# Kernel tuning notes

Measured on AMD Instinct MI355X. Metric: run time of the kernel, lower is better.

## Reference

```python
import jax, jax.numpy as jnp
import numpy as np

LEAK = 0.2
EPS_LN = 1e-5   # nn.LayerNorm default
EPS_IN = 1e-5   # nn.InstanceNorm2d default
EPS_D = 1e-8    # demodulation eps


def _leaky(x):
    return jnp.where(x >= 0, x, LEAK * x)


def _layernorm(s, g, b):
    mu = s.mean(-1, keepdims=True)
    v = ((s - mu) ** 2).mean(-1, keepdims=True)
    return (s - mu) / jnp.sqrt(v + EPS_LN) * g + b


def _instnorm(x):
    # per (b, c) normalization over HW, no affine (InstanceNorm2d default)
    mu = x.mean((2, 3), keepdims=True)
    v = ((x - mu) ** 2).mean((2, 3), keepdims=True)
    return (x - mu) / jnp.sqrt(v + EPS_IN)


def _conv(x, wt, pad):
    # x: [B,C,H,W], wt: [O,I,k,k]
    return jax.lax.conv_general_dilated(
        x, wt, (1, 1), [(pad, pad), (pad, pad)],
        dimension_numbers=('NCHW', 'OIHW', 'NCHW'))


def _modconv(x, w, wt, scale, mw, mb, lg, lb, asw, asb, abw, abb, demod):
    # style -> per-sample per-in-channel modulation
    s = _leaky(_layernorm(w @ mw.T + mb, lg, lb))              # [b, in]
    wb = wt[None] * (s[:, None, :, None, None] * scale[None])  # [b, O, I, k, k]
    # AdaIN on the input (use_adain=True in this block)
    sc = (w @ asw.T + asb)[:, :, None, None]
    bi = (w @ abw.T + abb)[:, :, None, None]
    x = sc * _instnorm(x) + bi
    if demod:
        d = jax.lax.rsqrt(jnp.sum(wb * wb, axis=(2, 3, 4)) + EPS_D)  # [b, O]
        wb = wb * d[:, :, None, None, None]
    pad = wt.shape[-1] // 2
    # per-sample conv == groups=b grouped conv in the torch original
    return jax.vmap(lambda xi, wi: _conv(xi[None], wi, pad)[0])(x, wb)


def _upsample2x(x):
    B, C, H, W = x.shape
    # bilinear, half-pixel centers == torch align_corners=False
    return jax.image.resize(x, (B, C, 2 * H, 2 * W), 'bilinear')


def setup_inputs() -> dict:
    key = jax.random.key(0)
    ks = iter(jax.random.split(key, 64))
    B, Cin, Cout, L, H = 8, 128, 64, 512, 128
    rn = lambda shape, s=1.0: jax.random.normal(next(ks), shape, jnp.float32) * s
    lin = 1.0 / float(np.sqrt(L))
    return dict(
        x=rn((B, Cin, H, H)), w=rn((B, L)),
        w1=rn((Cout, Cin, 3, 3), 0.02), sc1=jnp.ones((1, Cin, 1, 1), jnp.float32),
        m1_w=rn((Cin, L), lin), m1_b=jnp.zeros((Cin,), jnp.float32),
        ln1_g=jnp.ones((Cin,), jnp.float32), ln1_b=jnp.zeros((Cin,), jnp.float32),
        a1_sw=rn((Cin, L), lin), a1_sb=jnp.zeros((Cin,), jnp.float32),
        a1_bw=rn((Cin, L), lin), a1_bb=jnp.zeros((Cin,), jnp.float32),
        w25=rn((4, Cout, Cout, 3, 3), 0.02), sc25=jnp.ones((4, 1, Cout, 1, 1), jnp.float32),
        m25_w=rn((4, Cout, L), lin), m25_b=jnp.zeros((4, Cout), jnp.float32),
        ln25_g=jnp.ones((4, Cout), jnp.float32), ln25_b=jnp.zeros((4, Cout), jnp.float32),
        a25_sw=rn((4, Cout, L), lin), a25_sb=jnp.zeros((4, Cout), jnp.float32),
        a25_bw=rn((4, Cout, L), lin), a25_bb=jnp.zeros((4, Cout), jnp.float32),
        wr=rn((3, Cout, 1, 1), 0.02), scr=jnp.ones((1, Cout, 1, 1), jnp.float32),
        mr_w=rn((Cout, L), lin), mr_b=jnp.zeros((Cout,), jnp.float32),
        lnr_g=jnp.ones((Cout,), jnp.float32), lnr_b=jnp.zeros((Cout,), jnp.float32),
        ar_sw=rn((Cout, L), lin), ar_sb=jnp.zeros((Cout,), jnp.float32),
        ar_bw=rn((Cout, L), lin), ar_bb=jnp.zeros((Cout,), jnp.float32),
        sk_w=rn((Cout, Cin, 1, 1), 0.02), sk_b=jnp.zeros((Cout,), jnp.float32),
    )


def reference(x, w, w1, sc1, m1_w, m1_b, ln1_g, ln1_b, a1_sw, a1_sb, a1_bw, a1_bb,
              w25, sc25, m25_w, m25_b, ln25_g, ln25_b, a25_sw, a25_sb, a25_bw, a25_bb,
              wr, scr, mr_w, mr_b, lnr_g, lnr_b, ar_sw, ar_sb, ar_bw, ar_bb,
              sk_w, sk_b):
    x = _upsample2x(x)
    skip = _conv(x, sk_w, 0) + sk_b[None, :, None, None]
    h = _leaky(_modconv(x, w, w1, sc1, m1_w, m1_b, ln1_g, ln1_b,
                        a1_sw, a1_sb, a1_bw, a1_bb, True))
    for i in range(4):  # conv2..conv5, identical structure
        h = _leaky(_modconv(h, w, w25[i], sc25[i], m25_w[i], m25_b[i],
                            ln25_g[i], ln25_b[i], a25_sw[i], a25_sb[i],
                            a25_bw[i], a25_bb[i], True))
    h = h + skip
    rgb = _modconv(h, w, wr, scr, mr_w, mr_b, lnr_g, lnr_b,
                   ar_sw, ar_sb, ar_bw, ar_bb, False)
    return h, rgb
```

## Files before the change

kernel.cpp:

```cpp
#include <hip/hip_runtime.h>
#include <cstdint>

#define LEAK 0.2f

typedef __attribute__((ext_vector_type(8))) short bf16x8;
typedef __attribute__((ext_vector_type(4))) float f32x4;

__device__ __forceinline__ float leaky(float v){ return v >= 0.f ? v : LEAK*v; }

__device__ __forceinline__ uint32_t f32_to_bf16_rne(float v){
    uint32_t u = __float_as_uint(v);
    return (u + 0x7fffu + ((u >> 16) & 1u)) >> 16;
}
__device__ __forceinline__ uint32_t split_pack(float v){
    uint32_t u = __float_as_uint(v);
    uint32_t hb = (u + 0x7fffu + ((u >> 16) & 1u)) & 0xffff0000u;
    float lof = v - __uint_as_float(hb);
    uint32_t lo = f32_to_bf16_rne(lof);
    return (hb >> 16) | (lo << 16);
}

__global__ __launch_bounds__(128)
void style_all_kernel(const float* __restrict__ w,
    const float* __restrict__ m1_w,  const float* __restrict__ m1_b,
    const float* __restrict__ ln1_g, const float* __restrict__ ln1_b,
    const float* __restrict__ a1_sw, const float* __restrict__ a1_sb,
    const float* __restrict__ a1_bw, const float* __restrict__ a1_bb,
    const float* __restrict__ sc1,
    const float* __restrict__ m25_w,  const float* __restrict__ m25_b,
    const float* __restrict__ ln25_g, const float* __restrict__ ln25_b,
    const float* __restrict__ a25_sw, const float* __restrict__ a25_sb,
    const float* __restrict__ a25_bw, const float* __restrict__ a25_bb,
    const float* __restrict__ sc25,
    const float* __restrict__ mr_w,  const float* __restrict__ mr_b,
    const float* __restrict__ lnr_g, const float* __restrict__ lnr_b,
    const float* __restrict__ ar_sw, const float* __restrict__ ar_sb,
    const float* __restrict__ ar_bw, const float* __restrict__ ar_bb,
    const float* __restrict__ scr,
    float* __restrict__ sty)
{
    int l = blockIdx.x >> 3;
    int b = blockIdx.x & 7;
    const float *mw, *mb, *lng, *lnb, *asw, *asb, *abw, *abb, *sc;
    int Cin;
    if (l == 0) {
        mw=m1_w; mb=m1_b; lng=ln1_g; lnb=ln1_b;
        asw=a1_sw; asb=a1_sb; abw=a1_bw; abb=a1_bb; sc=sc1; Cin=128;
    } else if (l <= 4) {
        int j = l - 1;
        mw=m25_w+(size_t)j*32768; mb=m25_b+j*64; lng=ln25_g+j*64; lnb=ln25_b+j*64;
        asw=a25_sw+(size_t)j*32768; asb=a25_sb+j*64;
        abw=a25_bw+(size_t)j*32768; abb=a25_bb+j*64; sc=sc25+j*64; Cin=64;
    } else {
        mw=mr_w; mb=mr_b; lng=lnr_g; lnb=lnr_b;
        asw=ar_sw; asb=ar_sb; abw=ar_bw; abb=ar_bb; sc=scr; Cin=64;
    }
    float* out_sm  = sty + l*3072;
    float* out_asc = out_sm + 1024;
    float* out_abi = out_sm + 2048;

    __shared__ float wl[512];
    __shared__ float red[128];
    int tid = threadIdx.x;
    for (int j = tid; j < 512; j += 128) wl[j] = w[b*512 + j];
    __syncthreads();

    float t = 0.f, ascv = 0.f, abiv = 0.f;
    if (tid < Cin) {
        const float* r1 = mw  + (size_t)tid*512;
        const float* r2 = asw + (size_t)tid*512;
        const float* r3 = abw + (size_t)tid*512;
        for (int j = 0; j < 512; ++j) {
            float wj = wl[j];
            t    = fmaf(wj, r1[j], t);
            ascv = fmaf(wj, r2[j], ascv);
            abiv = fmaf(wj, r3[j], abiv);
        }
        t += mb[tid]; ascv += asb[tid]; abiv += abb[tid];
    }
    red[tid] = (tid < Cin) ? t : 0.f;
    __syncthreads();
    for (int s = 64; s > 0; s >>= 1) { if (tid < s) red[tid] += red[tid+s]; __syncthreads(); }
    float mu = red[0] / (float)Cin;
    __syncthreads();
    float dv = (tid < Cin) ? (t - mu) : 0.f;
    red[tid] = dv*dv;
    __syncthreads();
    for (int s = 64; s > 0; s >>= 1) { if (tid < s) red[tid] += red[tid+s]; __syncthreads(); }
    float var = red[0] / (float)Cin;
    float rstd = rsqrtf(var + 1e-5f);
    if (tid < Cin) {
        float sln = (t - mu) * rstd * lng[tid] + lnb[tid];
        sln = leaky(sln);
        out_sm[b*128 + tid]  = sln * sc[tid];
        out_asc[b*128 + tid] = ascv;
        out_abi[b*128 + tid] = abiv;
    }
}

__global__ __launch_bounds__(256)
void upsample_pack_kernel(const float* __restrict__ x, uint32_t* __restrict__ Up,
                          float* __restrict__ sums)
{
    int bid = blockIdx.x;
    int b = bid >> 8, y = bid & 255;
    int tid = threadIdx.x;
    int c = tid & 15, pg = tid >> 4;
    int q = y >> 1; int rlo, rhi; float wlo, whi;
    if (y & 1) { rlo = q; rhi = (q+1 < 127) ? q+1 : 127; wlo = 0.75f; whi = 0.25f; }
    else       { rlo = (q-1 > 0) ? q-1 : 0; rhi = q;     wlo = 0.25f; whi = 0.75f; }
    __shared__ float xs[2][16][129];
    __shared__ float red2[2][4][16];
    for (int cg = 0; cg < 8; ++cg) {
        __syncthreads();
        for (int e = tid; e < 4096; e += 256) {
            int row = e >> 11, cc = (e >> 7) & 15, px = e & 127;
            xs[row][cc][px] = x[((size_t)(b*128 + cg*16 + cc) << 14) + (row ? rhi : rlo)*128 + px];
        }
        __syncthreads();
        float s = 0.f, sq = 0.f;
        uint32_t* base = Up + ((((size_t)(b*8 + cg)*256 + y)*256))*16 + c;
        #pragma unroll
        for (int k = 0; k < 16; ++k) {
            int px = pg*16 + k;
            int m = px >> 1;
            float v;
            if (px & 1) {
                int m2 = (m+1 < 127) ? m+1 : 127;
                float vc = wlo*xs[0][c][m]  + whi*xs[1][c][m];
                float vr = wlo*xs[0][c][m2] + whi*xs[1][c][m2];
                v = 0.75f*vc + 0.25f*vr;
            } else {
                int m0 = (m-1 > 0) ? m-1 : 0;
                float vl = wlo*xs[0][c][m0] + whi*xs[1][c][m0];
                float vc = wlo*xs[0][c][m]  + whi*xs[1][c][m];
                v = 0.25f*vl + 0.75f*vc;
            }
            s += v; sq += v*v;
            base[(size_t)px*16] = split_pack(v);
        }
        s  += __shfl_xor(s, 16);  s  += __shfl_xor(s, 32);
        sq += __shfl_xor(sq, 16); sq += __shfl_xor(sq, 32);
        int wid = tid >> 6;
        if ((tid & 63) < 16) { red2[0][wid][c] = s; red2[1][wid][c] = sq; }
        __syncthreads();
        if (tid < 16) {
            float S = red2[0][0][tid] + red2[0][1][tid] + red2[0][2][tid] + red2[0][3][tid];
            float Q = red2[1][0][tid] + red2[1][1][tid] + red2[1][2][tid] + red2[1][3][tid];
            atomicAdd(&sums[(b*128 + cg*16 + tid)*2],     S);
            atomicAdd(&sums[(b*128 + cg*16 + tid)*2 + 1], Q);
        }
    }
}

__global__ __launch_bounds__(256)
void packskip_kernel(const float* __restrict__ skw, uint16_t* __restrict__ skp)
{
    int e = blockIdx.x*256 + threadIdx.x;
    if (e >= 8192) return;
    int o = e >> 7, i = e & 127;
    uint32_t pk = split_pack(skw[e]);
    int ic = i >> 4, cl = i & 15, cg = cl >> 2, j2 = (cl & 3)*2;
    uint16_t* dst = skp + ic*2048 + (o >> 4)*512 + cg*128 + (o & 15)*8 + j2;
    dst[0] = (uint16_t)(pk & 0xffffu);
    dst[1] = (uint16_t)(pk >> 16);
}

template<int CIN>
__global__ __launch_bounds__(CIN)
void packw_kernel(const float* __restrict__ wt, const float* __restrict__ sty,
                  const float* __restrict__ sums,
                  uint16_t* __restrict__ wp, float* __restrict__ bias9,
                  float* __restrict__ dmodL)
{
    int b = blockIdx.x >> 6;
    int o = blockIdx.x & 63;
    int i = threadIdx.x;

    float sm = sty[b*128 + i];
    float av = sty[1024 + b*128 + i];
    float bv = sty[2048 + b*128 + i];
    float s0 = sums[(b*CIN + i)*2], s1 = sums[(b*CIN + i)*2 + 1];
    float m = s0 * (1.f/65536.f);
    float var = s1 * (1.f/65536.f) - m*m;
    float r = rsqrtf((var > 0.f ? var : 0.f) + 1e-5f);
    float A  = sm * av * r;
    float Bv = sm * (bv - av*m*r);

    const float* wrow = wt + ((size_t)o*CIN + i)*9;
    float c9[9];
    #pragma unroll
    for (int k = 0; k < 9; ++k) c9[k] = wrow[k];

    const int NCH = CIN/16;
    int ic = i >> 4, cl = i & 15, cg = cl >> 2, j2 = (cl & 3)*2;
    uint16_t* wpb = wp + ((size_t)b*NCH + ic)*18432;
    float wsq = 0.f;
    #pragma unroll
    for (int k = 0; k < 9; ++k) { wsq = fmaf(c9[k], c9[k], wsq); }
    #pragma unroll
    for (int k = 0; k < 9; ++k) {
        float wv = c9[k] * A;
        uint32_t pk = split_pack(wv);
        uint16_t* dst = wpb + k*2048 + (o >> 4)*512 + cg*128 + (o & 15)*8 + j2;
        dst[0] = (uint16_t)(pk & 0xffffu);
        dst[1] = (uint16_t)(pk >> 16);
    }

    float colS[3][3];
    #pragma unroll
    for (int ky = 0; ky < 3; ++ky) {
        colS[ky][0] = c9[ky*3+1] + c9[ky*3+2];
        colS[ky][1] = c9[ky*3+0] + c9[ky*3+1] + c9[ky*3+2];
        colS[ky][2] = c9[ky*3+0] + c9[ky*3+1];
    }
    float part[9];
    #pragma unroll
    for (int rx = 0; rx < 3; ++rx) {
        part[0*3+rx] = colS[1][rx] + colS[2][rx];
        part[1*3+rx] = colS[0][rx] + colS[1][rx] + colS[2][rx];
        part[2*3+rx] = colS[0][rx] + colS[1][rx];
    }
    __shared__ float red[10][CIN];
    #pragma unroll
    for (int t = 0; t < 9; ++t) red[t][i] = part[t] * Bv;
    red[9][i] = wsq * sm * sm;
    __syncthreads();
    for (int s = CIN/2; s > 0; s >>= 1) {
        if (i < s) {
            #pragma unroll
            for (int t = 0; t < 10; ++t) red[t][i] += red[t][i + s];
        }
        __syncthreads();
    }
    if (i < 9) bias9[((size_t)(b*64 + o))*9 + i] = red[i][0];
    if (i == 9) dmodL[b*64 + o] = rsqrtf(red[9][0] + 1e-8f);
}

template<int CIN, int MODE, bool SKIP>
__global__ __launch_bounds__(512)
void conv_mfma_kernel(const uint32_t* __restrict__ inPair,
                      const uint16_t* __restrict__ Wp,
                      const float* __restrict__ bias9,
                      const float* __restrict__ dmod,
                      const uint16_t* __restrict__ skp,
                      const float* __restrict__ skb,
                      float* __restrict__ skipOut,
                      uint32_t* __restrict__ outPair,
                      float* __restrict__ outF32,
                      float* __restrict__ statsH)
{
    __shared__ __align__(16) unsigned char LDS[41600];
    const int tid = threadIdx.x;
    const int lane = tid & 63, wv = tid >> 6;
    const int rw = wv >> 2, oq = wv & 3;

    int bid = blockIdx.x;
    bid = (bid & 7) * 256 + (bid >> 3);
    const int xh = bid & 1, yb = (bid >> 1) & 127, b = bid >> 8;
    const int y0 = yb*2, x0 = xh*128;

    union U8 { uint32_t u[4]; bf16x8 v; };

    f32x4 acc[8];
    f32x4 accS[SKIP ? 8 : 1];
    #pragma unroll
    for (int q = 0; q < 8; ++q) acc[q] = (f32x4){0.f, 0.f, 0.f, 0.f};
    if constexpr (SKIP) {
        #pragma unroll
        for (int q = 0; q < 8; ++q) accS[q] = (f32x4){0.f, 0.f, 0.f, 0.f};
    }

    const int NCH = CIN/16;
    for (int ic = 0; ic < NCH; ++ic) {
        for (int e = tid; e < 2080; e += 512) {
            int part = e & 3;
            int pr = e >> 2;
            int px = pr % 130, row = pr / 130;
            int yy = y0 - 1 + row, xx = x0 - 1 + px;
            uint4 v = {0u, 0u, 0u, 0u};
            if (yy >= 0 && yy < 256 && xx >= 0 && xx < 256)
                v = *reinterpret_cast<const uint4*>(
                    inPair + ((((size_t)b*NCH + ic)*256 + yy)*256 + xx)*16 + part*4);
            *reinterpret_cast<uint4*>(LDS + row*10400 + px*80 + part*16) = v;
        }
        __syncthreads();
        const uint16_t* wbase = Wp + ((size_t)b*NCH + ic)*18432
                              + oq*512 + (lane >> 4)*128 + (lane & 15)*8;
        #pragma unroll
        for (int tap = 0; tap < 9; ++tap) {
            const int dy1 = tap/3, dxm = tap % 3;
            uint4 wv4 = *reinterpret_cast<const uint4*>(wbase + tap*2048);
            U8 wa, wb;
            #pragma unroll
            for (int q = 0; q < 4; ++q) {
                uint32_t ww = (&wv4.x)[q];
                wa.u[q] = __builtin_amdgcn_perm(ww, ww, 0x01000100u);
                wb.u[q] = __builtin_amdgcn_perm(ww, ww, 0x03020302u);
            }
            U8 sa, sb;
            if constexpr (SKIP) {
                if (tap == 4) {
                    uint4 sfrag = *reinterpret_cast<const uint4*>(
                        skp + ic*2048 + oq*512 + (lane >> 4)*128 + (lane & 15)*8);
                    #pragma unroll
                    for (int q = 0; q < 4; ++q) {
                        uint32_t ww = (&sfrag.x)[q];
                        sa.u[q] = __builtin_amdgcn_perm(ww, ww, 0x01000100u);
                        sb.u[q] = __builtin_amdgcn_perm(ww, ww, 0x03020302u);
                    }
                }
            }
            const int rowbase = (rw + dy1)*10400 + (lane >> 4)*16 + ((lane & 15) + dxm)*80;
            #pragma unroll
            for (int xf = 0; xf < 8; ++xf) {
                bf16x8 bf = *reinterpret_cast<const bf16x8*>(LDS + rowbase + xf*1280);
                acc[xf] = __builtin_amdgcn_mfma_f32_16x16x32_bf16(wa.v, bf, acc[xf], 0, 0, 0);
                acc[xf] = __builtin_amdgcn_mfma_f32_16x16x32_bf16(wb.v, bf, acc[xf], 0, 0, 0);
                if constexpr (SKIP) {
                    if (tap == 4) {
                        accS[xf] = __builtin_amdgcn_mfma_f32_16x16x32_bf16(sa.v, bf, accS[xf], 0, 0, 0);
                        accS[xf] = __builtin_amdgcn_mfma_f32_16x16x32_bf16(sb.v, bf, accS[xf], 0, 0, 0);
                    }
                }
            }
        }
        __syncthreads();
    }

    const int y = y0 + rw;
    const int ry = (y == 0) ? 0 : ((y == 255) ? 2 : 1);
    float dv4[4], bmid[4], bl[4], br[4], skb4[4];
    #pragma unroll
    for (int r2 = 0; r2 < 4; ++r2) {
        int o = oq*16 + (lane >> 4)*4 + r2;
        dv4[r2] = dmod[b*64 + o];
        const float* bp = bias9 + ((size_t)(b*64 + o))*9 + ry*3;
        bmid[r2] = bp[1];
        bl[r2] = bmid[r2]; br[r2] = bmid[r2];
        if (x0 == 0   && (lane & 15) == 0)  bl[r2] = bp[0];
        if (x0 == 128 && (lane & 15) == 15) br[r2] = bp[2];
        if constexpr (SKIP) skb4[r2] = skb[o];
    }

    float s4[4] = {0.f,0.f,0.f,0.f}, q4[4] = {0.f,0.f,0.f,0.f};
    #pragma unroll
    for (int xf = 0; xf < 8; ++xf) {
        #pragma unroll
        for (int r2 = 0; r2 < 4; ++r2) {
            float bias = (xf == 0) ? bl[r2] : ((xf == 7) ? br[r2] : bmid[r2]);
            float v = (acc[xf][r2] + bias) * dv4[r2];
            v = leaky(v);
            acc[xf][r2] = v;
            if (MODE != 2) { s4[r2] += v; q4[r2] += v*v; }
        }
    }

    if constexpr (SKIP) {
        #pragma unroll
        for (int xf = 0; xf < 8; ++xf) {
            #pragma unroll
            for (int r2 = 0; r2 < 4; ++r2) {
                int o = oq*16 + (lane >> 4)*4 + r2;
                size_t addr = ((size_t)(b*64 + o))*65536 + (size_t)y*256 + x0 + xf*16 + (lane & 15);
                skipOut[addr] = accS[xf][r2] + skb4[r2];
            }
        }
    }

    if constexpr (MODE == 2) {
        #pragma unroll
        for (int xf = 0; xf < 8; ++xf) {
            #pragma unroll
            for (int r2 = 0; r2 < 4; ++r2) {
                int o = oq*16 + (lane >> 4)*4 + r2;
                size_t addr = ((size_t)(b*64 + o))*65536 + (size_t)y*256 + x0 + xf*16 + (lane & 15);
                float v = acc[xf][r2] + outF32[addr];
                outF32[addr] = v;
                s4[r2] += v; q4[r2] += v*v;
            }
        }
    }

    #pragma unroll
    for (int r2 = 0; r2 < 4; ++r2) {
        #pragma unroll
        for (int w = 1; w < 16; w <<= 1) {
            s4[r2] += __shfl_xor(s4[r2], w);
            q4[r2] += __shfl_xor(q4[r2], w);
        }
    }
    if ((lane & 15) == 0) {
        #pragma unroll
        for (int r2 = 0; r2 < 4; ++r2) {
            int o = oq*16 + (lane >> 4)*4 + r2;
            atomicAdd(&statsH[(b*64 + o)*2],     s4[r2]);
            atomicAdd(&statsH[(b*64 + o)*2 + 1], q4[r2]);
        }
    }

    if constexpr (MODE != 2) {
        uint32_t* outb = outPair + ((((size_t)b*4 + oq)*256 + y)*256 + x0)*16 + (lane >> 4)*4;
        #pragma unroll
        for (int xf = 0; xf < 8; ++xf) {
            int px = xf*16 + (lane & 15);
            uint4 pk4;
            pk4.x = split_pack(acc[xf][0]);
            pk4.y = split_pack(acc[xf][1]);
            pk4.z = split_pack(acc[xf][2]);
            pk4.w = split_pack(acc[xf][3]);
            *reinterpret_cast<uint4*>(outb + (size_t)px*16) = pk4;
        }
    }
}

__global__ __launch_bounds__(256)
void rgb_kernel(const float* __restrict__ h, const float* __restrict__ wr,
                const float* __restrict__ sty, const float* __restrict__ sums,
                float* __restrict__ rgb)
{
    __shared__ float A[64], Bc[64];
    __shared__ float wl[192];
    int bid = blockIdx.x;
    int b = bid >> 7;
    int px0 = (bid & 127) * 512;
    int tid = threadIdx.x;
    if (tid < 64) {
        float smv = sty[b*128 + tid];
        float av  = sty[1024 + b*128 + tid];
        float bv  = sty[2048 + b*128 + tid];
        float s0 = sums[(b*64 + tid)*2], s1 = sums[(b*64 + tid)*2 + 1];
        float m = s0 * (1.f/65536.f);
        float var = s1 * (1.f/65536.f) - m*m;
        float r = rsqrtf((var > 0.f ? var : 0.f) + 1e-5f);
        A[tid]  = smv * av * r;
        Bc[tid] = smv * (bv - av*m*r);
    }
    if (tid < 192) wl[tid] = wr[tid];
    __syncthreads();
    int pix = px0 + tid*2;
    const float* hp = h + (size_t)b*64*65536 + pix;
    float a0[3] = {0,0,0}, a1[3] = {0,0,0};
    for (int i = 0; i < 64; ++i) {
        float2 v = *reinterpret_cast<const float2*>(hp + (size_t)i*65536);
        float xi0 = fmaf(A[i], v.x, Bc[i]);
        float xi1 = fmaf(A[i], v.y, Bc[i]);
        #pragma unroll
        for (int o = 0; o < 3; ++o) {
            float wv = wl[o*64 + i];
            a0[o] = fmaf(wv, xi0, a0[o]);
            a1[o] = fmaf(wv, xi1, a1[o]);
        }
    }
    float* rp = rgb + (size_t)b*3*65536 + pix;
    #pragma unroll
    for (int o = 0; o < 3; ++o)
        *reinterpret_cast<float2*>(rp + (size_t)o*65536) = make_float2(a0[o], a1[o]);
}

extern "C" void kernel_launch(void* const* d_in, const int* in_sizes, int n_in,
                              void* d_out, int out_size, void* d_ws, size_t ws_size,
                              hipStream_t stream)
{
    const float* x     = (const float*)d_in[0];
    const float* w     = (const float*)d_in[1];
    const float* w1    = (const float*)d_in[2];
    const float* sc1   = (const float*)d_in[3];
    const float* m1_w  = (const float*)d_in[4];
    const float* m1_b  = (const float*)d_in[5];
    const float* ln1_g = (const float*)d_in[6];
    const float* ln1_b = (const float*)d_in[7];
    const float* a1_sw = (const float*)d_in[8];
    const float* a1_sb = (const float*)d_in[9];
    const float* a1_bw = (const float*)d_in[10];
    const float* a1_bb = (const float*)d_in[11];
    const float* w25   = (const float*)d_in[12];
    const float* sc25  = (const float*)d_in[13];
    const float* m25_w = (const float*)d_in[14];
    const float* m25_b = (const float*)d_in[15];
    const float* ln25_g= (const float*)d_in[16];
    const float* ln25_b= (const float*)d_in[17];
    const float* a25_sw= (const float*)d_in[18];
    const float* a25_sb= (const float*)d_in[19];
    const float* a25_bw= (const float*)d_in[20];
    const float* a25_bb= (const float*)d_in[21];
    const float* wr    = (const float*)d_in[22];
    const float* scr   = (const float*)d_in[23];
    const float* mr_w  = (const float*)d_in[24];
    const float* mr_b  = (const float*)d_in[25];
    const float* lnr_g = (const float*)d_in[26];
    const float* lnr_b = (const float*)d_in[27];
    const float* ar_sw = (const float*)d_in[28];
    const float* ar_sb = (const float*)d_in[29];
    const float* ar_bw = (const float*)d_in[30];
    const float* ar_bb = (const float*)d_in[31];
    const float* sk_w  = (const float*)d_in[32];
    const float* sk_b  = (const float*)d_in[33];

    float* outp    = (float*)d_out;
    float* h_out   = outp;
    float* rgb_out = outp + (size_t)33554432;

    uint8_t* ws = (uint8_t*)d_ws;
    uint32_t*  Upair  = (uint32_t*)(ws + 0);
    uint32_t*  hpB    = (uint32_t*)(ws + 0);
    uint32_t*  hpA    = (uint32_t*)(ws + 268435456ull);
    uint16_t*  WpBase = (uint16_t*)(ws + 402653184ull);
    float*     sty    = (float*)(ws + 409731072ull);
    float*     dmod   = (float*)(ws + 409804800ull);
    float*     stats  = (float*)(ws + 409815040ull);
    float*     bias9  = (float*)(ws + 409843712ull);
    uint16_t*  skp    = (uint16_t*)(ws + 409935872ull);

    float* sumsU = stats;
    float* st1   = stats + 2048;
    float* st2   = stats + 3072;
    float* st3   = stats + 4096;
    float* st4   = stats + 5120;
    float* st5   = stats + 6144;

    uint16_t* Wp1 = WpBase;
    uint16_t* Wp2 = WpBase + 1179648;
    uint16_t* Wp3 = Wp2 + 589824;
    uint16_t* Wp4 = Wp3 + 589824;
    uint16_t* Wp5 = Wp4 + 589824;

    hipMemsetAsync(stats, 0, 28672, stream);

    style_all_kernel<<<48,128,0,stream>>>(w,
        m1_w, m1_b, ln1_g, ln1_b, a1_sw, a1_sb, a1_bw, a1_bb, sc1,
        m25_w, m25_b, ln25_g, ln25_b, a25_sw, a25_sb, a25_bw, a25_bb, sc25,
        mr_w, mr_b, lnr_g, lnr_b, ar_sw, ar_sb, ar_bw, ar_bb, scr,
        sty);

    packskip_kernel<<<32,256,0,stream>>>(sk_w, skp);

    upsample_pack_kernel<<<2048,256,0,stream>>>(x, Upair, sumsU);

    packw_kernel<128><<<512,128,0,stream>>>(w1, sty, sumsU, Wp1, bias9, dmod);
    conv_mfma_kernel<128,1,true><<<2048,512,0,stream>>>(Upair, Wp1, bias9, dmod,
                                                        skp, sk_b, h_out,
                                                        hpA, nullptr, st1);
    packw_kernel<64><<<512,64,0,stream>>>(w25, sty + 3072, st1, Wp2, bias9 + 4608, dmod + 512);
    conv_mfma_kernel<64,1,false><<<2048,512,0,stream>>>(hpA, Wp2, bias9 + 4608, dmod + 512,
                                                        nullptr, nullptr, nullptr,
                                                        hpB, nullptr, st2);
    packw_kernel<64><<<512,64,0,stream>>>(w25 + 36864, sty + 2*3072, st2, Wp3, bias9 + 2*4608, dmod + 2*512);
    conv_mfma_kernel<64,1,false><<<2048,512,0,stream>>>(hpB, Wp3, bias9 + 2*4608, dmod + 2*512,
                                                        nullptr, nullptr, nullptr,
                                                        hpA, nullptr, st3);
    packw_kernel<64><<<512,64,0,stream>>>(w25 + 2*36864, sty + 3*3072, st3, Wp4, bias9 + 3*4608, dmod + 3*512);
    conv_mfma_kernel<64,1,false><<<2048,512,0,stream>>>(hpA, Wp4, bias9 + 3*4608, dmod + 3*512,
                                                        nullptr, nullptr, nullptr,
                                                        hpB, nullptr, st4);
    packw_kernel<64><<<512,64,0,stream>>>(w25 + 3*36864, sty + 4*3072, st4, Wp5, bias9 + 4*4608, dmod + 4*512);
    conv_mfma_kernel<64,2,false><<<2048,512,0,stream>>>(hpB, Wp5, bias9 + 4*4608, dmod + 4*512,
                                                        nullptr, nullptr, nullptr,
                                                        nullptr, h_out, st5);

    rgb_kernel<<<1024,256,0,stream>>>(h_out, wr, sty + 5*3072, st5, rgb_out);
}
```

Before: 1.325 ms.

## Add dedicated mid-layer conv kernel with 2-row tiles and multi-fragment register blocking

Adds a specialized conv kernel for the four 64-channel mid layers. Each block handles two rows by half-width, and each wave accumulates a 4x2 grid of MFMA fragments, so each weight load and LDS B-fragment is reused across more outputs. The input halo is staged per 16-channel group into padded LDS. The cost is more accumulator registers and possible occupancy loss at 512 threads, plus a changed block-to-tile mapping.

```diff
diff --git a/kernel.cpp b/kernel.cpp
--- a/kernel.cpp
+++ b/kernel.cpp
@@ -410,6 +410,175 @@
             pk4.z = split_pack(acc[xf][2]);
             pk4.w = split_pack(acc[xf][3]);
             *reinterpret_cast<uint4*>(outb + (size_t)px*16) = pk4;
+        }
+    }
+}
+
+template<int MODE>
+__global__ __launch_bounds__(512)
+void conv_mid_kernel(const uint32_t* __restrict__ inPair,
+                     const uint16_t* __restrict__ Wp,
+                     const float* __restrict__ bias9,
+                     const float* __restrict__ dmod,
+                     uint32_t* __restrict__ outPair,
+                     float* __restrict__ outF32,
+                     float* __restrict__ statsH)
+{
+    __shared__ __align__(16) unsigned char LDS[41600];
+    const int tid = threadIdx.x;
+    const int lane = tid & 63, wvi = tid >> 6;
+    const int rw = wvi >> 2, xh = (wvi >> 1) & 1, oh = wvi & 1;
+
+    int bid = blockIdx.x;
+    bid = (bid & 7) * 256 + (bid >> 3);
+    const int xhb = bid & 1, yb = (bid >> 1) & 127, b = bid >> 8;
+    const int y0 = yb*2, x0 = xhb*128;
+
+    union U8 { uint32_t u[4]; bf16x8 v; };
+
+    f32x4 acc[4][2];
+    #pragma unroll
+    for (int xfl = 0; xfl < 4; ++xfl) {
+        acc[xfl][0] = (f32x4){0.f, 0.f, 0.f, 0.f};
+        acc[xfl][1] = (f32x4){0.f, 0.f, 0.f, 0.f};
+    }
+
+    for (int ic = 0; ic < 4; ++ic) {
+        for (int e = tid; e < 2080; e += 512) {
+            int part = e & 3;
+            int pr = e >> 2;
+            int px = pr % 130, row = pr / 130;
+            int yy = y0 - 1 + row, xx = x0 - 1 + px;
+            uint4 v = {0u, 0u, 0u, 0u};
+            if (yy >= 0 && yy < 256 && xx >= 0 && xx < 256)
+                v = *reinterpret_cast<const uint4*>(
+                    inPair + ((((size_t)b*4 + ic)*256 + yy)*256 + xx)*16 + part*4);
+            *reinterpret_cast<uint4*>(LDS + row*10400 + px*80 + part*16) = v;
+        }
+        __syncthreads();
+        const uint16_t* wbase = Wp + ((size_t)b*4 + ic)*18432
+                              + (lane >> 4)*128 + (lane & 15)*8;
+        #pragma unroll
+        for (int tap = 0; tap < 9; ++tap) {
+            const int dy1 = tap/3, dxm = tap % 3;
+            uint4 w0 = *reinterpret_cast<const uint4*>(wbase + tap*2048 + (oh*2+0)*512);
+            uint4 w1 = *reinterpret_cast<const uint4*>(wbase + tap*2048 + (oh*2+1)*512);
+            U8 wa0, wb0, wa1, wb1;
+            #pragma unroll
+            for (int q = 0; q < 4; ++q) {
+                uint32_t u0 = (&w0.x)[q], u1 = (&w1.x)[q];
+                wa0.u[q] = __builtin_amdgcn_perm(u0, u0, 0x01000100u);
+                wb0.u[q] = __builtin_amdgcn_perm(u0, u0, 0x03020302u);
+                wa1.u[q] = __builtin_amdgcn_perm(u1, u1, 0x01000100u);
+                wb1.u[q] = __builtin_amdgcn_perm(u1, u1, 0x03020302u);
+            }
+            const int rowbase = (rw + dy1)*10400 + (lane >> 4)*16
+                              + ((lane & 15) + xh*64 + dxm)*80;
+            bf16x8 bfv[4];
+            #pragma unroll
+            for (int xfl = 0; xfl < 4; ++xfl)
+                bfv[xfl] = *reinterpret_cast<const bf16x8*>(LDS + rowbase + xfl*1280);
+            #pragma unroll
+            for (int xfl = 0; xfl < 4; ++xfl)
+                acc[xfl][0] = __builtin_amdgcn_mfma_f32_16x16x32_bf16(wa0.v, bfv[xfl], acc[xfl][0], 0, 0, 0);
+            #pragma unroll
+            for (int xfl = 0; xfl < 4; ++xfl)
+                acc[xfl][1] = __builtin_amdgcn_mfma_f32_16x16x32_bf16(wa1.v, bfv[xfl], acc[xfl][1], 0, 0, 0);
+            #pragma unroll
+            for (int xfl = 0; xfl < 4; ++xfl)
+                acc[xfl][0] = __builtin_amdgcn_mfma_f32_16x16x32_bf16(wb0.v, bfv[xfl], acc[xfl][0], 0, 0, 0);
+            #pragma unroll
+            for (int xfl = 0; xfl < 4; ++xfl)
+                acc[xfl][1] = __builtin_amdgcn_mfma_f32_16x16x32_bf16(wb1.v, bfv[xfl], acc[xfl][1], 0, 0, 0);
+        }
+        __syncthreads();
+    }
+
+    const int y = y0 + rw;
+    const int ry = (y == 0) ? 0 : ((y == 255) ? 2 : 1);
+    float dv4[2][4], bmid[2][4], bl4[2][4], br4[2][4];
+    #pragma unroll
+    for (int ofl = 0; ofl < 2; ++ofl)
+        #pragma unroll
+        for (int r2 = 0; r2 < 4; ++r2) {
+            int o = (oh*2+ofl)*16 + (lane >> 4)*4 + r2;
+            dv4[ofl][r2] = dmod[b*64 + o];
+            const float* bp = bias9 + ((size_t)(b*64 + o))*9 + ry*3;
+            bmid[ofl][r2] = bp[1];
+            bl4[ofl][r2] = bmid[ofl][r2]; br4[ofl][r2] = bmid[ofl][r2];
+            if (x0 == 0   && xh == 0 && (lane & 15) == 0)  bl4[ofl][r2] = bp[0];
+            if (x0 == 128 && xh == 1 && (lane & 15) == 15) br4[ofl][r2] = bp[2];
+        }
+
+    float s4[2][4] = {{0.f,0.f,0.f,0.f},{0.f,0.f,0.f,0.f}};
+    float q4[2][4] = {{0.f,0.f,0.f,0.f},{0.f,0.f,0.f,0.f}};
+    #pragma unroll
+    for (int xfl = 0; xfl < 4; ++xfl) {
+        bool isL = (xh == 0 && xfl == 0), isR = (xh == 1 && xfl == 3);
+        #pragma unroll
+        for (int ofl = 0; ofl < 2; ++ofl)
+            #pragma unroll
+            for (int r2 = 0; r2 < 4; ++r2) {
+                float bias = isL ? bl4[ofl][r2] : (isR ? br4[ofl][r2] : bmid[ofl][r2]);
+                float v = (acc[xfl][ofl][r2] + bias) * dv4[ofl][r2];
+                v = leaky(v);
+                acc[xfl][ofl][r2] = v;
+                if (MODE != 2) { s4[ofl][r2] += v; q4[ofl][r2] += v*v; }
+            }
+    }
+
+    if constexpr (MODE == 2) {
+        #pragma unroll
+        for (int xfl = 0; xfl < 4; ++xfl)
+            #pragma unroll
+            for (int ofl = 0; ofl < 2; ++ofl)
+                #pragma unroll
+                for (int r2 = 0; r2 < 4; ++r2) {
+                    int o = (oh*2+ofl)*16 + (lane >> 4)*4 + r2;
+                    size_t addr = ((size_t)(b*64 + o))*65536 + (size_t)y*256
+                                + x0 + xh*64 + xfl*16 + (lane & 15);
+                    float v = acc[xfl][ofl][r2] + outF32[addr];
+                    outF32[addr] = v;
+                    s4[ofl][r2] += v; q4[ofl][r2] += v*v;
+                }
+    }
+
+    #pragma unroll
+    for (int ofl = 0; ofl < 2; ++ofl)
+        #pragma unroll
+        for (int r2 = 0; r2 < 4; ++r2) {
+            #pragma unroll
+            for (int w = 1; w < 16; w <<= 1) {
+                s4[ofl][r2] += __shfl_xor(s4[ofl][r2], w);
+                q4[ofl][r2] += __shfl_xor(q4[ofl][r2], w);
+            }
+        }
+    if ((lane & 15) == 0) {
+        #pragma unroll
+        for (int ofl = 0; ofl < 2; ++ofl)
+            #pragma unroll
+            for (int r2 = 0; r2 < 4; ++r2) {
+                int o = (oh*2+ofl)*16 + (lane >> 4)*4 + r2;
+                atomicAdd(&statsH[(b*64 + o)*2],     s4[ofl][r2]);
+                atomicAdd(&statsH[(b*64 + o)*2 + 1], q4[ofl][r2]);
+            }
+    }
+
+    if constexpr (MODE != 2) {
+        #pragma unroll
+        for (int ofl = 0; ofl < 2; ++ofl) {
+            uint32_t* outb = outPair + ((((size_t)b*4 + oh*2+ofl)*256 + y)*256 + x0 + xh*64)*16
+                           + (lane >> 4)*4;
+            #pragma unroll
+            for (int xfl = 0; xfl < 4; ++xfl) {
+                int px = xfl*16 + (lane & 15);
+                uint4 pk4;
+                pk4.x = split_pack(acc[xfl][ofl][0]);
+                pk4.y = split_pack(acc[xfl][ofl][1]);
+                pk4.z = split_pack(acc[xfl][ofl][2]);
+                pk4.w = split_pack(acc[xfl][ofl][3]);
+                *reinterpret_cast<uint4*>(outb + (size_t)px*16) = pk4;
+            }
         }
     }
 }
@@ -542,21 +711,17 @@
                                                         skp, sk_b, h_out,
                                                         hpA, nullptr, st1);
     packw_kernel<64><<<512,64,0,stream>>>(w25, sty + 3072, st1, Wp2, bias9 + 4608, dmod + 512);
-    conv_mfma_kernel<64,1,false><<<2048,512,0,stream>>>(hpA, Wp2, bias9 + 4608, dmod + 512,
-                                                        nullptr, nullptr, nullptr,
-                                                        hpB, nullptr, st2);
+    conv_mid_kernel<1><<<2048,512,0,stream>>>(hpA, Wp2, bias9 + 4608, dmod + 512,
+                                              hpB, nullptr, st2);
     packw_kernel<64><<<512,64,0,stream>>>(w25 + 36864, sty + 2*3072, st2, Wp3, bias9 + 2*4608, dmod + 2*512);
-    conv_mfma_kernel<64,1,false><<<2048,512,0,stream>>>(hpB, Wp3, bias9 + 2*4608, dmod + 2*512,
-                                                        nullptr, nullptr, nullptr,
-                                                        hpA, nullptr, st3);
+    conv_mid_kernel<1><<<2048,512,0,stream>>>(hpB, Wp3, bias9 + 2*4608, dmod + 2*512,
+                                              hpA, nullptr, st3);
     packw_kernel<64><<<512,64,0,stream>>>(w25 + 2*36864, sty + 3*3072, st3, Wp4, bias9 + 3*4608, dmod + 3*512);
-    conv_mfma_kernel<64,1,false><<<2048,512,0,stream>>>(hpA, Wp4, bias9 + 3*4608, dmod + 3*512,
-                                                        nullptr, nullptr, nullptr,
-                                                        hpB, nullptr, st4);
+    conv_mid_kernel<1><<<2048,512,0,stream>>>(hpA, Wp4, bias9 + 3*4608, dmod + 3*512,
+                                              hpB, nullptr, st4);
     packw_kernel<64><<<512,64,0,stream>>>(w25 + 3*36864, sty + 4*3072, st4, Wp5, bias9 + 4*4608, dmod + 4*512);
-    conv_mfma_kernel<64,2,false><<<2048,512,0,stream>>>(hpB, Wp5, bias9 + 4*4608, dmod + 4*512,
-                                                        nullptr, nullptr, nullptr,
-                                                        nullptr, h_out, st5);
+    conv_mid_kernel<2><<<2048,512,0,stream>>>(hpB, Wp5, bias9 + 4*4608, dmod + 4*512,
+                                              nullptr, h_out, st5);
 
     rgb_kernel<<<1024,256,0,stream>>>(h_out, wr, sty + 5*3072, st5, rgb_out);
 }
```

Result: slower. 1.692 ms (+27.7%).
